# Performance work log

Hardware: AMD Instinct MI355X
Metric: run time of the kernel (lower is better)

Reference implementation:

```python
import jax, jax.numpy as jnp
import numpy as np

TEMPERATURE = 0.07
EPS = 1e-12  # matches F.normalize eps clamp


def setup_inputs() -> dict:
    key = jax.random.key(0)
    k1, k2 = jax.random.split(key)
    B, S, D = 8, 512, 128
    return {
        "z_i": jax.random.normal(k1, (B, S, D), dtype=jnp.float32),
        "z_j": jax.random.normal(k2, (B, S, D), dtype=jnp.float32),
    }


def reference(z_i, z_j):
    D = z_i.shape[-1]
    zi = z_i.reshape(-1, D)  # [N, D]
    zj = z_j.reshape(-1, D)
    # cosine normalization (use_cosine_similarity=True)
    zi = zi / jnp.maximum(jnp.linalg.norm(zi, axis=1, keepdims=True), EPS)
    zj = zj / jnp.maximum(jnp.linalg.norm(zj, axis=1, keepdims=True), EPS)
    N = zi.shape[0]
    z = jnp.concatenate([zi, zj], axis=0)  # [2N, D]
    sim = (z @ z.T) / TEMPERATURE  # [2N, 2N]
    # denominator: logsumexp over all j != i (positives + negatives)
    diag = jnp.eye(2 * N, dtype=bool)
    lse = jax.nn.logsumexp(jnp.where(diag, -jnp.inf, sim), axis=1)  # [2N]
    # positive logit for row i is sim[i, (i+N) mod 2N] = <zi, zj>/T for both halves
    pos_half = jnp.sum(zi * zj, axis=1) / TEMPERATURE  # [N]
    pos = jnp.concatenate([pos_half, pos_half])  # [2N]
    return jnp.mean(-pos + lse)
```

## Files before the change

kernel.cpp:

```cpp
#include <hip/hip_runtime.h>
#include <stdint.h>


#define TOTAL   8192
#define NHALF   4096
#define DK      128
#define TEMP_INV 14.285714285714286f
#define SCALE    4.539816f
#define TILE    128

typedef short  bf16x8  __attribute__((ext_vector_type(8)));
typedef float  floatx4 __attribute__((ext_vector_type(4)));

#if __has_builtin(__builtin_amdgcn_exp2f)
#define EXP2(x) __builtin_amdgcn_exp2f(x)
#else
#define EXP2(x) exp2f(x)
#endif

__device__ __forceinline__ uint32_t f2bf(float f) {
  uint32_t u = __float_as_uint(f);
  return (u + 0x7fffu + ((u >> 16) & 1u)) >> 16;
}
__device__ __forceinline__ uint32_t pack2bf(float lo, float hi) {
  return f2bf(lo) | (f2bf(hi) << 16);
}

__global__ __launch_bounds__(256) void ntx_norm(
    const float* __restrict__ zi, const float* __restrict__ zj,
    uint32_t* __restrict__ zn,
    float* __restrict__ pos,
    float* __restrict__ rowsum)
{
  const int t = threadIdx.x;
  if (blockIdx.x < 32) rowsum[blockIdx.x * 256 + t] = 0.0f;

  const int wave = t >> 6, lane = t & 63;
  const int i = blockIdx.x * 4 + wave;

  const float2 vi = *(const float2*)(zi + (size_t)i * DK + lane * 2);
  const float2 vj = *(const float2*)(zj + (size_t)i * DK + lane * 2);
  float ssi = vi.x * vi.x + vi.y * vi.y;
  float ssj = vj.x * vj.x + vj.y * vj.y;
  float dij = vi.x * vj.x + vi.y * vj.y;
#pragma unroll
  for (int m = 1; m <= 32; m <<= 1) {
    ssi += __shfl_xor(ssi, m, 64);
    ssj += __shfl_xor(ssj, m, 64);
    dij += __shfl_xor(dij, m, 64);
  }
  const float invi = 1.0f / fmaxf(sqrtf(ssi), 1e-12f);
  const float invj = 1.0f / fmaxf(sqrtf(ssj), 1e-12f);

  zn[(size_t)i * 64 + lane] =
      pack2bf(vi.x * invi * SCALE, vi.y * invi * SCALE);
  zn[(size_t)(i + NHALF) * 64 + lane] =
      pack2bf(vj.x * invj * SCALE, vj.y * invj * SCALE);
  if (lane == 0) pos[i] = dij * invi * invj * TEMP_INV;
}

__global__ __launch_bounds__(256, 4) void ntx_gemm(
    const uint16_t* __restrict__ z,
    float* __restrict__ rowsum)
{
  const int bi = blockIdx.x, bj = blockIdx.y;
  if (bj < bi) return;

  __shared__ uint4 lb4[TILE * 17];

  const int t = threadIdx.x;
  const int wave = t >> 6, lane = t & 63;
  const int q = lane >> 4, c = lane & 15;
  const int I0 = bi * TILE, J0 = bj * TILE;
  const int rowbase = I0 + wave * 32;
  const bool diagblk = (bi == bj);

  {
    const int ch = t & 15, r0 = t >> 4;
#pragma unroll
    for (int p = 0; p < 8; ++p) {
      const int r = r0 + p * 16;
      lb4[r * 17 + ch] = *(const uint4*)(z + (size_t)(J0 + r) * DK + ch * 8);
    }
  }

  bf16x8 afrag[2][4];
#pragma unroll
  for (int s = 0; s < 2; ++s) {
    const uint16_t* ap = z + (size_t)(rowbase + s * 16 + c) * DK + q * 8;
#pragma unroll
    for (int kk = 0; kk < 4; ++kk)
      afrag[s][kk] = *(const bf16x8*)(ap + kk * 32);
  }

  float runsum[2][4] = {{0.f, 0.f, 0.f, 0.f}, {0.f, 0.f, 0.f, 0.f}};
  float colacc[8];

  __syncthreads();

#pragma unroll
  for (int jt = 0; jt < 8; ++jt) {
    bf16x8 bfrag[4];
#pragma unroll
    for (int kk = 0; kk < 4; ++kk)
      bfrag[kk] = *(const bf16x8*)&lb4[(jt * 16 + c) * 17 + kk * 4 + q];

    float cpart = 0.0f;
#pragma unroll
    for (int s = 0; s < 2; ++s) {
      floatx4 acc = {0.0f, 0.0f, 0.0f, 0.0f};
#pragma unroll
      for (int kk = 0; kk < 4; ++kk)
        acc = __builtin_amdgcn_mfma_f32_16x16x32_bf16(afrag[s][kk],
                                                      bfrag[kk], acc, 0, 0, 0);
      if (diagblk && (jt == wave * 2 + s)) {
#pragma unroll
        for (int r = 0; r < 4; ++r) {
          float e = EXP2(acc[r]);
          e = (q * 4 + r == c) ? 0.0f : e;
          runsum[s][r] += e;
          cpart += e;
        }
      } else {
#pragma unroll
        for (int r = 0; r < 4; ++r) {
          float e = EXP2(acc[r]);
          runsum[s][r] += e;
          cpart += e;
        }
      }
    }
    cpart += __shfl_xor(cpart, 16, 64);
    cpart += __shfl_xor(cpart, 32, 64);
    colacc[jt] = cpart;
  }

#pragma unroll
  for (int s = 0; s < 2; ++s)
#pragma unroll
    for (int r = 0; r < 4; ++r) {
      float v = runsum[s][r];
      v += __shfl_xor(v, 1, 64);
      v += __shfl_xor(v, 2, 64);
      v += __shfl_xor(v, 4, 64);
      v += __shfl_xor(v, 8, 64);
      runsum[s][r] = v;
    }
  if (c == 0) {
#pragma unroll
    for (int s = 0; s < 2; ++s)
#pragma unroll
      for (int r = 0; r < 4; ++r)
        atomicAdd(&rowsum[rowbase + s * 16 + q * 4 + r], runsum[s][r]);
  }
  if (!diagblk && q == 0) {
#pragma unroll
    for (int jt = 0; jt < 8; ++jt)
      atomicAdd(&rowsum[J0 + jt * 16 + c], colacc[jt]);
  }
}

__global__ __launch_bounds__(1024) void ntx_final(
    const float* __restrict__ rowsum, const float* __restrict__ pos,
    float* __restrict__ out)
{
  const int t = threadIdx.x;
  float acc = 0.0f;
  for (int r = t; r < TOTAL; r += 1024) acc += __logf(rowsum[r]);
  for (int r = t; r < NHALF; r += 1024) acc -= 2.0f * pos[r];
#pragma unroll
  for (int m = 1; m <= 32; m <<= 1) acc += __shfl_xor(acc, m, 64);
  __shared__ float red[16];
  const int wave = t >> 6, lane = t & 63;
  if (lane == 0) red[wave] = acc;
  __syncthreads();
  if (t == 0) {
    float s = 0.0f;
#pragma unroll
    for (int w = 0; w < 16; ++w) s += red[w];
    out[0] = s / (float)TOTAL;
  }
}

extern "C" void kernel_launch(void* const* d_in, const int* in_sizes, int n_in,
                              void* d_out, int out_size, void* d_ws,
                              size_t ws_size, hipStream_t stream) {
  const float* zi = (const float*)d_in[0];
  const float* zj = (const float*)d_in[1];
  float* out = (float*)d_out;

  char* ws = (char*)d_ws;
  uint16_t* zn     = (uint16_t*)ws;
  float*    rowsum = (float*)(ws + (size_t)TOTAL * DK * 2);
  float*    pos    = (float*)(ws + (size_t)TOTAL * DK * 2 + TOTAL * 4);

  ntx_norm<<<dim3(NHALF / 4), dim3(256), 0, stream>>>(zi, zj, (uint32_t*)zn,
                                                      pos, rowsum);
  ntx_gemm<<<dim3(64, 64), dim3(256), 0, stream>>>(zn, rowsum);
  ntx_final<<<dim3(1), dim3(1024), 0, stream>>>(rowsum, pos, out);
}
```

Baseline: 93.79 us.

## Replace symmetric tiled GEMM with full row-split GEMM writing per-split partials

Gives up the upper-triangle symmetry trick, LDS staging and column-sum atomics. Each block now handles 128 rows against a 512-column chunk, reading B fragments straight from global/L2, and writes per-split row sums without atomics. The final kernel becomes multi-block, summing the partials and reducing into the output with an atomicAdd. This removes the atomics, the empty lower-triangle blocks and the LDS syncs, but roughly doubles MFMA and exp work and relies on L2 for the B operand reloads.

```diff
diff --git a/kernel.cpp b/kernel.cpp
--- a/kernel.cpp
+++ b/kernel.cpp
@@ -7,7 +7,9 @@
 #define DK      128
 #define TEMP_INV 14.285714285714286f
 #define SCALE    4.539816f
-#define TILE    128
+#define JSPLITS 16
+#define JCHUNK  512
+#define IROWS   128
 
 typedef short  bf16x8  __attribute__((ext_vector_type(8)));
 typedef float  floatx4 __attribute__((ext_vector_type(4)));
@@ -30,10 +32,10 @@
     const float* __restrict__ zi, const float* __restrict__ zj,
     uint32_t* __restrict__ zn,
     float* __restrict__ pos,
-    float* __restrict__ rowsum)
+    float* __restrict__ out)
 {
   const int t = threadIdx.x;
-  if (blockIdx.x < 32) rowsum[blockIdx.x * 256 + t] = 0.0f;
+  if (blockIdx.x == 0 && t == 0) out[0] = 0.0f;
 
   const int wave = t >> 6, lane = t & 63;
   const int i = blockIdx.x * 4 + wave;
@@ -61,28 +63,14 @@
 
 __global__ __launch_bounds__(256, 4) void ntx_gemm(
     const uint16_t* __restrict__ z,
-    float* __restrict__ rowsum)
+    float* __restrict__ partial)
 {
-  const int bi = blockIdx.x, bj = blockIdx.y;
-  if (bj < bi) return;
-
-  __shared__ uint4 lb4[TILE * 17];
-
   const int t = threadIdx.x;
   const int wave = t >> 6, lane = t & 63;
   const int q = lane >> 4, c = lane & 15;
-  const int I0 = bi * TILE, J0 = bj * TILE;
+  const int I0 = blockIdx.x * IROWS;
+  const int J0 = blockIdx.y * JCHUNK;
   const int rowbase = I0 + wave * 32;
-  const bool diagblk = (bi == bj);
-
-  {
-    const int ch = t & 15, r0 = t >> 4;
-#pragma unroll
-    for (int p = 0; p < 8; ++p) {
-      const int r = r0 + p * 16;
-      lb4[r * 17 + ch] = *(const uint4*)(z + (size_t)(J0 + r) * DK + ch * 8);
-    }
-  }
 
   bf16x8 afrag[2][4];
 #pragma unroll
@@ -94,18 +82,16 @@
   }
 
   float runsum[2][4] = {{0.f, 0.f, 0.f, 0.f}, {0.f, 0.f, 0.f, 0.f}};
-  float colacc[8];
 
-  __syncthreads();
-
-#pragma unroll
-  for (int jt = 0; jt < 8; ++jt) {
+#pragma unroll 2
+  for (int jt = 0; jt < JCHUNK / 16; ++jt) {
+    const int jc = J0 + jt * 16;
+    const uint16_t* bp = z + (size_t)(jc + c) * DK + q * 8;
     bf16x8 bfrag[4];
 #pragma unroll
     for (int kk = 0; kk < 4; ++kk)
-      bfrag[kk] = *(const bf16x8*)&lb4[(jt * 16 + c) * 17 + kk * 4 + q];
+      bfrag[kk] = *(const bf16x8*)(bp + kk * 32);
 
-    float cpart = 0.0f;
 #pragma unroll
     for (int s = 0; s < 2; ++s) {
       floatx4 acc = {0.0f, 0.0f, 0.0f, 0.0f};
@@ -113,26 +99,18 @@
       for (int kk = 0; kk < 4; ++kk)
         acc = __builtin_amdgcn_mfma_f32_16x16x32_bf16(afrag[s][kk],
                                                       bfrag[kk], acc, 0, 0, 0);
-      if (diagblk && (jt == wave * 2 + s)) {
+      const int rb = rowbase + s * 16;
+      if (jc == rb) {
 #pragma unroll
         for (int r = 0; r < 4; ++r) {
           float e = EXP2(acc[r]);
-          e = (q * 4 + r == c) ? 0.0f : e;
-          runsum[s][r] += e;
-          cpart += e;
+          runsum[s][r] += (q * 4 + r == c) ? 0.0f : e;
         }
       } else {
 #pragma unroll
-        for (int r = 0; r < 4; ++r) {
-          float e = EXP2(acc[r]);
-          runsum[s][r] += e;
-          cpart += e;
-        }
+        for (int r = 0; r < 4; ++r) runsum[s][r] += EXP2(acc[r]);
       }
     }
-    cpart += __shfl_xor(cpart, 16, 64);
-    cpart += __shfl_xor(cpart, 32, 64);
-    colacc[jt] = cpart;
   }
 
 #pragma unroll
@@ -151,34 +129,31 @@
     for (int s = 0; s < 2; ++s)
 #pragma unroll
       for (int r = 0; r < 4; ++r)
-        atomicAdd(&rowsum[rowbase + s * 16 + q * 4 + r], runsum[s][r]);
-  }
-  if (!diagblk && q == 0) {
-#pragma unroll
-    for (int jt = 0; jt < 8; ++jt)
-      atomicAdd(&rowsum[J0 + jt * 16 + c], colacc[jt]);
+        partial[(size_t)blockIdx.y * TOTAL + rowbase + s * 16 + q * 4 + r] =
+            runsum[s][r];
   }
 }
 
-__global__ __launch_bounds__(1024) void ntx_final(
-    const float* __restrict__ rowsum, const float* __restrict__ pos,
+__global__ __launch_bounds__(256) void ntx_final(
+    const float* __restrict__ partial, const float* __restrict__ pos,
     float* __restrict__ out)
 {
-  const int t = threadIdx.x;
-  float acc = 0.0f;
-  for (int r = t; r < TOTAL; r += 1024) acc += __logf(rowsum[r]);
-  for (int r = t; r < NHALF; r += 1024) acc -= 2.0f * pos[r];
+  const int r = blockIdx.x * 256 + threadIdx.x;
+  float s = 0.0f;
+#pragma unroll
+  for (int p = 0; p < JSPLITS; ++p) s += partial[(size_t)p * TOTAL + r];
+  float acc = __logf(s);
+  if (r < NHALF) acc -= 2.0f * pos[r];
+
 #pragma unroll
   for (int m = 1; m <= 32; m <<= 1) acc += __shfl_xor(acc, m, 64);
-  __shared__ float red[16];
-  const int wave = t >> 6, lane = t & 63;
+  __shared__ float red[4];
+  const int wave = threadIdx.x >> 6, lane = threadIdx.x & 63;
   if (lane == 0) red[wave] = acc;
   __syncthreads();
-  if (t == 0) {
-    float s = 0.0f;
-#pragma unroll
-    for (int w = 0; w < 16; ++w) s += red[w];
-    out[0] = s / (float)TOTAL;
+  if (threadIdx.x == 0) {
+    float b = red[0] + red[1] + red[2] + red[3];
+    atomicAdd(out, b * (1.0f / (float)TOTAL));
   }
 }
 
@@ -190,12 +165,13 @@
   float* out = (float*)d_out;
 
   char* ws = (char*)d_ws;
-  uint16_t* zn     = (uint16_t*)ws;
-  float*    rowsum = (float*)(ws + (size_t)TOTAL * DK * 2);
-  float*    pos    = (float*)(ws + (size_t)TOTAL * DK * 2 + TOTAL * 4);
+  uint16_t* zn      = (uint16_t*)ws;
+  float*    partial = (float*)(ws + (size_t)TOTAL * DK * 2);
+  float*    pos     = (float*)(ws + (size_t)TOTAL * DK * 2 +
+                               (size_t)JSPLITS * TOTAL * 4);
 
   ntx_norm<<<dim3(NHALF / 4), dim3(256), 0, stream>>>(zi, zj, (uint32_t*)zn,
-                                                      pos, rowsum);
-  ntx_gemm<<<dim3(64, 64), dim3(256), 0, stream>>>(zn, rowsum);
-  ntx_final<<<dim3(1), dim3(1024), 0, stream>>>(rowsum, pos, out);
+                                                      pos, out);
+  ntx_gemm<<<dim3(TOTAL / IROWS, JSPLITS), dim3(256), 0, stream>>>(zn, partial);
+  ntx_final<<<dim3(TOTAL / 256), dim3(256), 0, stream>>>(partial, pos, out);
 }
```

Result: slower. 123.3 us (+31.5%).
